# Kernel optimization log

Measured on AMD Instinct MI355X. Metric: run time of the kernel, lower is better.

## Reference

```python
import jax, jax.numpy as jnp
import numpy as np

D_MODEL = 1024
HEAD = 16
D_K = D_MODEL // HEAD
NEG_INF = -1.0e9


def setup_inputs() -> dict:
    key = jax.random.key(0)
    ks = jax.random.split(key, 12)
    B, S = 2, 2048
    scale = 1.0 / np.sqrt(D_MODEL)
    inp = {
        "query": jax.random.normal(ks[0], (B, S, D_MODEL), jnp.float32),
        "key": jax.random.normal(ks[1], (B, S, D_MODEL), jnp.float32),
        "value": jax.random.normal(ks[2], (B, S, D_MODEL), jnp.float32),
        "mask": jax.random.randint(ks[3], (B, 1, 1, S), 0, 2, jnp.int32),
        "Wq": jax.random.normal(ks[4], (D_MODEL, D_MODEL), jnp.float32) * scale,
        "bq": jnp.zeros((D_MODEL,), jnp.float32),
        "Wk": jax.random.normal(ks[5], (D_MODEL, D_MODEL), jnp.float32) * scale,
        "bk": jnp.zeros((D_MODEL,), jnp.float32),
        "Wv": jax.random.normal(ks[6], (D_MODEL, D_MODEL), jnp.float32) * scale,
        "bv": jnp.zeros((D_MODEL,), jnp.float32),
        "Wo": jax.random.normal(ks[7], (D_MODEL, D_MODEL), jnp.float32) * scale,
        "bo": jnp.zeros((D_MODEL,), jnp.float32),
    }
    return inp


def reference(query, key, value, mask, Wq, bq, Wk, bk, Wv, bv, Wo, bo):
    B, S, _ = query.shape
    # QKV projections (torch nn.Linear: x @ W^T + b)
    q = query @ Wq.T + bq
    k = key @ Wk.T + bk
    v = value @ Wv.T + bv
    # [B, H, S, d_k]
    q = q.reshape(B, S, HEAD, D_K).transpose(0, 2, 1, 3)
    k = k.reshape(B, S, HEAD, D_K).transpose(0, 2, 1, 3)
    v = v.reshape(B, S, HEAD, D_K).transpose(0, 2, 1, 3)
    # scores [B, H, S, S]
    scores = jnp.einsum("bhqd,bhkd->bhqk", q, k) / jnp.sqrt(jnp.float32(D_K))
    scores = jnp.where(mask == 0, jnp.float32(NEG_INF), scores)
    attn = jax.nn.softmax(scores, axis=-1)  # dropout off (eval mode)
    ctx = jnp.einsum("bhqk,bhkd->bhqd", attn, v)
    ctx = ctx.transpose(0, 2, 1, 3).reshape(B, S, D_MODEL)
    return ctx @ Wo.T + bo
```

## Files before the change

kernel.cpp:

```cpp
#include <hip/hip_runtime.h>
#include <cstdint>
#include <cstddef>

typedef unsigned short u16;
typedef unsigned int   u32;
typedef __bf16 bf16x8 __attribute__((ext_vector_type(8)));
typedef float  f32x4  __attribute__((ext_vector_type(4)));

#define D_MODEL 1024
#define SEQ     2048
#define NTOK    4096
#define NHEAD   16
#define DK      64

__device__ __forceinline__ float fast_exp2(float x) {
  return __builtin_amdgcn_exp2f(x);
}

__device__ __forceinline__ u16 f2bf(float f) {
  u32 u = __builtin_bit_cast(u32, f);
  u += 0x7fffu + ((u >> 16) & 1u);
  return (u16)(u >> 16);
}

__device__ __forceinline__ void gload16(const u16* g, u16* l) {
  __builtin_amdgcn_global_load_lds(
      (__attribute__((address_space(1))) void*)(uintptr_t)g,
      (__attribute__((address_space(3))) void*)l,
      16, 0, 0);
}

__global__ __launch_bounds__(256) void mask_scan(const int* __restrict__ mask,
                                                 int* __restrict__ idx,
                                                 int* __restrict__ cnt) {
  const int b = blockIdx.x, t = threadIdx.x;
  const int lane = t & 63, w = t >> 6;
  __shared__ int sW[4];
  __shared__ int sTot;
  int m8[8];
  const int base = b * SEQ + t * 8;
  int tot = 0;
#pragma unroll
  for (int i = 0; i < 8; ++i) {
    m8[i] = (mask[base + i] != 0);
    tot += m8[i];
  }
  int v = tot;
#pragma unroll
  for (int d = 1; d < 64; d <<= 1) {
    int u = __shfl_up(v, d);
    if (lane >= d) v += u;
  }
  if (lane == 63) sW[w] = v;
  __syncthreads();
  if (t == 0) {
    int run = 0;
#pragma unroll
    for (int i = 0; i < 4; ++i) { int tmp = sW[i]; sW[i] = run; run += tmp; }
    sTot = run;
  }
  __syncthreads();
  int pos = v - tot + sW[w];
#pragma unroll
  for (int i = 0; i < 8; ++i)
    if (m8[i]) idx[b * SEQ + pos++] = t * 8 + i;
  const int cn = sTot;
  if (t == 0) cnt[b] = cn;
  for (int j = cn + t; j < SEQ; j += 256) idx[b * SEQ + j] = 0;
}

__global__ __launch_bounds__(256) void w_convert(
    const float* __restrict__ wq, const float* __restrict__ wk,
    const float* __restrict__ wv, const float* __restrict__ wo,
    u16* __restrict__ wb) {
  const int total = 1 << 20;
  for (int cid = blockIdx.x * blockDim.x + threadIdx.x; cid < total;
       cid += gridDim.x * blockDim.x) {
    int which = cid >> 18;
    int off = cid & ((1 << 18) - 1);
    const float* src = which == 0 ? wq : (which == 1 ? wk : (which == 2 ? wv : wo));
    u16* dst = wb + ((size_t)which << 20);
    float4 f = ((const float4*)src)[off];
    ushort4 u;
    u.x = f2bf(f.x); u.y = f2bf(f.y); u.z = f2bf(f.z); u.w = f2bf(f.w);
    ((ushort4*)dst)[off] = u;
  }
}

__global__ __launch_bounds__(256, 3) void gemm_qkv(
    const float* __restrict__ Aq, const float* __restrict__ Ak,
    const float* __restrict__ Av, const u16* __restrict__ Bw,
    const float* __restrict__ b0, const float* __restrict__ b1,
    const float* __restrict__ b2, u16* __restrict__ Cout) {
  __shared__ __align__(16) u16 smem[3 * 128 * 64];
  u16* sA = smem;

  const int t = threadIdx.x;
  const int z = blockIdx.z;
  const float* Ap = (z == 0) ? Aq : ((z == 1) ? Ak : Av);
  const u16* Bp = Bw + ((size_t)z << 20);
  const float* bias = (z == 0) ? b0 : ((z == 1) ? b1 : b2);
  const float scl = (z == 0) ? 0.18033688011f : 1.0f;

  const int m0 = blockIdx.x * 128, n0 = blockIdx.y * 128;
  const int lane = t & 63, wv = t >> 6;
  const int wm = (wv >> 1) * 64, wn = (wv & 1) * 64;
  const int c = lane & 15, qd = lane >> 4;

  const int arow = t >> 3;
  const int aoff = (((t & 7) - arow) & 7) * 8;
  const float* gaA = Ap + (size_t)(m0 + arow) * D_MODEL + aoff;
  const u16* gaB = Bp + (size_t)(n0 + arow) * D_MODEL + aoff;

  float4 pa[4][2];
#pragma unroll
  for (int j = 0; j < 4; ++j) {
    pa[j][0] = *(const float4*)(gaA + (size_t)(32 * j) * D_MODEL);
    pa[j][1] = *(const float4*)(gaA + (size_t)(32 * j) * D_MODEL + 4);
  }
#pragma unroll
  for (int j = 0; j < 4; ++j)
    gload16(gaB + (size_t)(32 * j) * D_MODEL, smem + 8192 + (t + 256 * j) * 8);

  f32x4 acc[4][4] = {};

  for (int kbi = 0; kbi < 16; ++kbi) {
    const int cur = kbi & 1;
    __syncthreads();
#pragma unroll
    for (int j = 0; j < 4; ++j) {
      u32 w[4];
#pragma unroll
      for (int h2 = 0; h2 < 2; ++h2) {
        float4 f = pa[j][h2];
        w[2 * h2] = (u32)f2bf(f.x) | ((u32)f2bf(f.y) << 16);
        w[2 * h2 + 1] = (u32)f2bf(f.z) | ((u32)f2bf(f.w) << 16);
      }
      uint4 v4 = {w[0], w[1], w[2], w[3]};
      *(uint4*)&sA[(t + 256 * j) * 8] = v4;
    }
    __syncthreads();
    if (kbi + 1 < 16) {
      const int kb2 = (kbi + 1) * 64;
      u16* sBn = smem + 8192 + (1 - cur) * 8192;
#pragma unroll
      for (int j = 0; j < 4; ++j)
        gload16(gaB + kb2 + (size_t)(32 * j) * D_MODEL, sBn + (t + 256 * j) * 8);
#pragma unroll
      for (int j = 0; j < 4; ++j) {
        pa[j][0] = *(const float4*)(gaA + kb2 + (size_t)(32 * j) * D_MODEL);
        pa[j][1] = *(const float4*)(gaA + kb2 + (size_t)(32 * j) * D_MODEL + 4);
      }
    }
    const u16* sB = smem + 8192 + cur * 8192;
#pragma unroll
    for (int s = 0; s < 2; ++s) {
      const int ao = ((s * 4 + qd + wm + c) & 7) * 8;
      const int bo = ((s * 4 + qd + wn + c) & 7) * 8;
      bf16x8 af[4], bfr[4];
#pragma unroll
      for (int i = 0; i < 4; ++i)
        af[i] = *(const bf16x8*)&sA[(wm + i * 16 + c) * 64 + ao];
#pragma unroll
      for (int j = 0; j < 4; ++j)
        bfr[j] = *(const bf16x8*)&sB[(wn + j * 16 + c) * 64 + bo];
#pragma unroll
      for (int i = 0; i < 4; ++i)
#pragma unroll
        for (int j = 0; j < 4; ++j)
          acc[i][j] = __builtin_amdgcn_mfma_f32_16x16x32_bf16(af[i], bfr[j],
                                                              acc[i][j], 0, 0, 0);
    }
  }
  __syncthreads();

  u16* sC = smem;
  if (z == 2) {
#pragma unroll
    for (int j = 0; j < 4; ++j) {
      const int col = wn + j * 16 + c;
      const float bv = bias[n0 + col];
#pragma unroll
      for (int i = 0; i < 4; ++i)
#pragma unroll
        for (int r = 0; r < 4; ++r)
          sC[col * 136 + wm + i * 16 + qd * 4 + r] = f2bf(acc[i][j][r] + bv);
    }
    __syncthreads();
    u16* VT = Cout + ((size_t)2 << 22);
    const int bb = m0 >> 11, s0 = m0 & 2047;
    const int sidx = (t & 15) * 8;
#pragma unroll
    for (int outer = 0; outer < 8; ++outer) {
      const int vrow = outer * 16 + (t >> 4);
      const int col = n0 + vrow;
      const int hh = col >> 6, dd = col & 63;
      uint4 val = *(const uint4*)&sC[vrow * 136 + sidx];
      *(uint4*)&VT[((size_t)((bb * NHEAD + hh) * DK + dd)) * SEQ + s0 + sidx] =
          val;
    }
  } else {
#pragma unroll
    for (int j = 0; j < 4; ++j) {
      const int col = wn + j * 16 + c;
      const float bv = bias[n0 + col];
#pragma unroll
      for (int i = 0; i < 4; ++i)
#pragma unroll
        for (int r = 0; r < 4; ++r)
          sC[(wm + i * 16 + qd * 4 + r) * 136 + col] =
              f2bf((acc[i][j][r] + bv) * scl);
    }
    __syncthreads();
    u16* outp = Cout + ((size_t)z << 22);
    const int cidx = (t & 15) * 8;
#pragma unroll
    for (int outer = 0; outer < 8; ++outer) {
      const int lrow = outer * 16 + (t >> 4);
      uint4 val = *(const uint4*)&sC[lrow * 136 + cidx];
      *(uint4*)&outp[(size_t)(m0 + lrow) * D_MODEL + n0 + cidx] = val;
    }
  }
}

__global__ __launch_bounds__(256) void vtc_gather(const u16* __restrict__ VT,
                                                  const int* __restrict__ idx,
                                                  const int* __restrict__ cnt,
                                                  u16* __restrict__ VTc) {
  const int row = blockIdx.x;
  const int b = row >> 10;
  const int cn = cnt[b];
  const u16* src = VT + (size_t)row * SEQ;
  u16* dst = VTc + (size_t)row * SEQ;
  const int* ib = idx + b * SEQ;
  for (int j = threadIdx.x; j < cn; j += 256) dst[j] = src[ib[j]];
}

__global__ __launch_bounds__(256) void mha_attn(
    const u16* __restrict__ QKVb, const u16* __restrict__ VTc,
    const int* __restrict__ idx, const int* __restrict__ cnt,
    u16* __restrict__ Opart, float* __restrict__ ml) {
  __shared__ __align__(16) u16 sK[64 * 72];
  __shared__ __align__(16) u16 sVt[64 * 72];
  __shared__ __align__(16) u16 sP[128 * 72];

  const int t = threadIdx.x, lane = t & 63, wq = t >> 6;
  const int c = lane & 15, qd = lane >> 4;
  const int qb = blockIdx.x, h = blockIdx.y;
  const int b = blockIdx.z & 1, ck = blockIdx.z >> 1;

  const int cn = cnt[b];
  const int nb = (cn + 63) >> 6;
  const int half = (nb + 1) >> 1;
  const int kstart = ck ? half : 0;
  const int kend = ck ? nb : half;

  const u16* Qg = QKVb;
  const u16* Kg = QKVb + ((size_t)4 << 20);
  const u16* VTch = VTc + ((size_t)((b * NHEAD + h) * DK)) * SEQ;
  const int rowbase = b * SEQ;
  const int colbase = h * DK;

  bf16x8 aq[2][2];
#pragma unroll
  for (int qt = 0; qt < 2; ++qt) {
    const u16* g = Qg +
                   (size_t)(rowbase + qb * 128 + wq * 32 + qt * 16 + c) * D_MODEL +
                   colbase + qd * 8;
    aq[qt][0] = *(const bf16x8*)g;
    aq[qt][1] = *(const bf16x8*)(g + 32);
  }

  float l[2] = {0.f, 0.f};
  f32x4 o[2][4] = {};
  const float MADD = -1.4426950e9f;
  const float MFIX = 16.0f;

  const int r0s = t >> 2, offs = (t & 3) * 16;
  const u16* gvb = VTch + (size_t)r0s * SEQ + offs;
  const int* idxb = idx + b * SEQ + r0s;

  uint4 k0, k1, v0, v1;
  int sNext2 = 0;
  if (kstart < kend) {
    const int s0i = idxb[kstart * 64];
    const u16* gk = Kg + (size_t)(rowbase + s0i) * D_MODEL + colbase + offs;
    const u16* gv = gvb + kstart * 64;
    k0 = *(const uint4*)gk;
    k1 = *(const uint4*)(gk + 8);
    v0 = *(const uint4*)gv;
    v1 = *(const uint4*)(gv + 8);
    if (kstart + 1 < kend) sNext2 = idxb[(kstart + 1) * 64];
  }

  for (int kbi = kstart; kbi < kend; ++kbi) {
    __syncthreads();
    *(uint4*)&sK[r0s * 72 + offs] = k0;
    *(uint4*)&sK[r0s * 72 + offs + 8] = k1;
    *(uint4*)&sVt[r0s * 72 + offs] = v0;
    *(uint4*)&sVt[r0s * 72 + offs + 8] = v1;
    __syncthreads();
    if (kbi + 1 < kend) {
      const u16* gk = Kg + (size_t)(rowbase + sNext2) * D_MODEL + colbase + offs;
      const u16* gv = gvb + (kbi + 1) * 64;
      k0 = *(const uint4*)gk;
      k1 = *(const uint4*)(gk + 8);
      v0 = *(const uint4*)gv;
      v1 = *(const uint4*)(gv + 8);
    }
    if (kbi + 2 < kend) sNext2 = idxb[(kbi + 2) * 64];

    const bool full = ((kbi + 1) << 6) <= cn;
    f32x4 st[2][4];
#pragma unroll
    for (int tt = 0; tt < 4; ++tt) {
      bf16x8 ak0 = *(const bf16x8*)&sK[(tt * 16 + c) * 72 + qd * 8];
      bf16x8 ak1 = *(const bf16x8*)&sK[(tt * 16 + c) * 72 + qd * 8 + 32];
      f32x4 cin;
      if (full) {
        cin = f32x4{0.f, 0.f, 0.f, 0.f};
      } else {
        const int jb = (kbi << 6) + tt * 16 + qd * 4;
        cin = f32x4{jb + 0 < cn ? 0.f : MADD, jb + 1 < cn ? 0.f : MADD,
                    jb + 2 < cn ? 0.f : MADD, jb + 3 < cn ? 0.f : MADD};
      }
#pragma unroll
      for (int qt = 0; qt < 2; ++qt) {
        f32x4 a =
            __builtin_amdgcn_mfma_f32_16x16x32_bf16(ak0, aq[qt][0], cin, 0, 0, 0);
        a = __builtin_amdgcn_mfma_f32_16x16x32_bf16(ak1, aq[qt][1], a, 0, 0, 0);
        st[qt][tt] = a;
      }
    }

#pragma unroll
    for (int qt = 0; qt < 2; ++qt) {
      float sum = 0.f;
      const int prow = (wq * 32 + qt * 16 + c) * 72;
#pragma unroll
      for (int tt = 0; tt < 4; ++tt) {
        u32 pk[2];
#pragma unroll
        for (int pr = 0; pr < 2; ++pr) {
          u32 p0 = __builtin_bit_cast(u32, fast_exp2(st[qt][tt][2 * pr] - MFIX));
          u32 p1 =
              __builtin_bit_cast(u32, fast_exp2(st[qt][tt][2 * pr + 1] - MFIX));
          u32 hi1 = p1 & 0xffff0000u;
          pk[pr] = (p0 >> 16) | hi1;
          sum += __builtin_bit_cast(float, p0 & 0xffff0000u);
          sum += __builtin_bit_cast(float, hi1);
        }
        uint2 pv2 = {pk[0], pk[1]};
        *(uint2*)&sP[prow + tt * 16 + qd * 4] = pv2;
      }
      l[qt] += sum;
    }

    bf16x8 bp[2][2];
#pragma unroll
    for (int qt = 0; qt < 2; ++qt) {
      const int prow = (wq * 32 + qt * 16 + c) * 72;
      bp[qt][0] = *(const bf16x8*)&sP[prow + qd * 8];
      bp[qt][1] = *(const bf16x8*)&sP[prow + qd * 8 + 32];
    }
#pragma unroll
    for (int dt = 0; dt < 4; ++dt) {
      bf16x8 av0 = *(const bf16x8*)&sVt[(dt * 16 + c) * 72 + qd * 8];
      bf16x8 av1 = *(const bf16x8*)&sVt[(dt * 16 + c) * 72 + qd * 8 + 32];
#pragma unroll
      for (int qt = 0; qt < 2; ++qt) {
        o[qt][dt] =
            __builtin_amdgcn_mfma_f32_16x16x32_bf16(av0, bp[qt][0], o[qt][dt], 0, 0, 0);
        o[qt][dt] =
            __builtin_amdgcn_mfma_f32_16x16x32_bf16(av1, bp[qt][1], o[qt][dt], 0, 0, 0);
      }
    }
  }

  const size_t obase =
      (size_t)ck * 4194304 + ((size_t)((b * NHEAD + h) * SEQ) + qb * 128) * 64;
  const int mlbase = ((ck * 2 + b) * NHEAD + h) * SEQ + qb * 128;
#pragma unroll
  for (int qt = 0; qt < 2; ++qt) {
    float ls = l[qt];
    ls += __shfl_xor(ls, 16);
    ls += __shfl_xor(ls, 32);
    const float inv = (ls != 0.f) ? 1.0f / ls : 0.f;
    const int q = wq * 32 + qt * 16 + c;
#pragma unroll
    for (int dt = 0; dt < 4; ++dt) {
      u32 lo = (u32)f2bf(o[qt][dt][0] * inv) |
               ((u32)f2bf(o[qt][dt][1] * inv) << 16);
      u32 hi = (u32)f2bf(o[qt][dt][2] * inv) |
               ((u32)f2bf(o[qt][dt][3] * inv) << 16);
      uint2 ov = {lo, hi};
      *(uint2*)&Opart[obase + (size_t)q * 64 + dt * 16 + qd * 4] = ov;
    }
    if (qd == 0) ml[mlbase + q] = ls;
  }
}

__global__ __launch_bounds__(256) void mha_combine(
    const u16* __restrict__ Opart, const float* __restrict__ ml,
    u16* __restrict__ ctx) {
  const int tid = blockIdx.x * 256 + threadIdx.x;
  const int row = tid >> 3, d0 = (tid & 7) * 8;
  const int b = row >> 15, h = (row >> 11) & 15, q = row & 2047;
  float l1 = ml[row];
  float l2 = ml[65536 + row];
  float inv = 1.0f / (l1 + l2);
  float w1 = l1 * inv, w2 = l2 * inv;
  const size_t o1 = (size_t)row * 64 + d0;
  uint4 pa = *(const uint4*)(Opart + o1);
  uint4 pb = *(const uint4*)(Opart + 4194304 + o1);
  u32 wa[4] = {pa.x, pa.y, pa.z, pa.w};
  u32 wb[4] = {pb.x, pb.y, pb.z, pb.w};
  u32 out[4];
#pragma unroll
  for (int j = 0; j < 4; ++j) {
    float alo = __builtin_bit_cast(float, wa[j] << 16);
    float ahi = __builtin_bit_cast(float, wa[j] & 0xffff0000u);
    float blo = __builtin_bit_cast(float, wb[j] << 16);
    float bhi = __builtin_bit_cast(float, wb[j] & 0xffff0000u);
    float rlo = w1 * alo + w2 * blo;
    float rhi = w1 * ahi + w2 * bhi;
    out[j] = (u32)f2bf(rlo) | ((u32)f2bf(rhi) << 16);
  }
  uint4 ov = {out[0], out[1], out[2], out[3]};
  *(uint4*)&ctx[((size_t)(b * SEQ + q)) * D_MODEL + h * DK + d0] = ov;
}

__global__ __launch_bounds__(256) void gemm_out(
    const u16* __restrict__ A, const u16* __restrict__ Bw,
    const float* __restrict__ bias, float* __restrict__ Cout) {
  __shared__ __align__(16) u16 sAb[2][128 * 64];
  __shared__ __align__(16) u16 sBc[2][64 * 64];

  const int t = threadIdx.x;
  const int m0 = blockIdx.x * 128, n0 = blockIdx.y * 64;
  const int lane = t & 63, wv = t >> 6;
  const int wm = (wv >> 1) * 64, wn = (wv & 1) * 32;
  const int c = lane & 15, qd = lane >> 4;

  const int arow = t >> 3;
  const int aoff = (((t & 7) - arow) & 7) * 8;
  const u16* gaA = A + (size_t)(m0 + arow) * D_MODEL + aoff;
  const u16* gaB = Bw + (size_t)(n0 + arow) * D_MODEL + aoff;

#pragma unroll
  for (int j = 0; j < 4; ++j)
    gload16(gaA + (size_t)(32 * j) * D_MODEL, &sAb[0][(t + 256 * j) * 8]);
#pragma unroll
  for (int j = 0; j < 2; ++j)
    gload16(gaB + (size_t)(32 * j) * D_MODEL, &sBc[0][(t + 256 * j) * 8]);

  f32x4 acc[4][2] = {};

  for (int kbi = 0; kbi < 16; ++kbi) {
    const int cur = kbi & 1;
    __syncthreads();
    if (kbi + 1 < 16) {
      const int kb2 = (kbi + 1) * 64;
#pragma unroll
      for (int j = 0; j < 4; ++j)
        gload16(gaA + kb2 + (size_t)(32 * j) * D_MODEL,
                &sAb[1 - cur][(t + 256 * j) * 8]);
#pragma unroll
      for (int j = 0; j < 2; ++j)
        gload16(gaB + kb2 + (size_t)(32 * j) * D_MODEL,
                &sBc[1 - cur][(t + 256 * j) * 8]);
    }
    const u16* sA = sAb[cur];
    const u16* sB = sBc[cur];
#pragma unroll
    for (int s = 0; s < 2; ++s) {
      const int ao = ((s * 4 + qd + wm + c) & 7) * 8;
      const int bo = ((s * 4 + qd + wn + c) & 7) * 8;
      bf16x8 af[4], bfr[2];
#pragma unroll
      for (int i = 0; i < 4; ++i)
        af[i] = *(const bf16x8*)&sA[(wm + i * 16 + c) * 64 + ao];
#pragma unroll
      for (int j = 0; j < 2; ++j)
        bfr[j] = *(const bf16x8*)&sB[(wn + j * 16 + c) * 64 + bo];
#pragma unroll
      for (int i = 0; i < 4; ++i)
#pragma unroll
        for (int j = 0; j < 2; ++j)
          acc[i][j] = __builtin_amdgcn_mfma_f32_16x16x32_bf16(af[i], bfr[j],
                                                              acc[i][j], 0, 0, 0);
    }
  }

#pragma unroll
  for (int j = 0; j < 2; ++j) {
    const int col = n0 + wn + j * 16 + c;
    const float bv = bias[col];
#pragma unroll
    for (int i = 0; i < 4; ++i)
#pragma unroll
      for (int r = 0; r < 4; ++r) {
        const int row = m0 + wm + i * 16 + qd * 4 + r;
        Cout[(size_t)row * D_MODEL + col] = acc[i][j][r] + bv;
      }
  }
}

extern "C" void kernel_launch(void* const* d_in, const int* in_sizes, int n_in,
                              void* d_out, int out_size, void* d_ws,
                              size_t ws_size, hipStream_t stream) {
  const float* query = (const float*)d_in[0];
  const float* key   = (const float*)d_in[1];
  const float* value = (const float*)d_in[2];
  const int*   mask  = (const int*)d_in[3];
  const float* Wq = (const float*)d_in[4];
  const float* bq = (const float*)d_in[5];
  const float* Wk = (const float*)d_in[6];
  const float* bk = (const float*)d_in[7];
  const float* Wv = (const float*)d_in[8];
  const float* bv = (const float*)d_in[9];
  const float* Wo = (const float*)d_in[10];
  const float* bo = (const float*)d_in[11];

  u16* ws  = (u16*)d_ws;
  u16* Wb  = ws + ((size_t)12 << 20);
  u16* QKV = ws + ((size_t)16 << 20);
  u16* CTX = ws + ((size_t)28 << 20);
  u16* VTc = ws;
  u16* Opart = ws + ((size_t)4 << 20);
  float* ml = (float*)(ws + ((size_t)12 << 20));
  int* idxp = (int*)(ws + ((size_t)28 << 20));
  int* cntp = idxp + 2 * SEQ;

  mask_scan<<<dim3(2), dim3(256), 0, stream>>>(mask, idxp, cntp);
  w_convert<<<dim3(1024), dim3(256), 0, stream>>>(Wq, Wk, Wv, Wo, Wb);
  gemm_qkv<<<dim3(32, 8, 3), dim3(256), 0, stream>>>(query, key, value, Wb, bq,
                                                     bk, bv, QKV);
  vtc_gather<<<dim3(2048), dim3(256), 0, stream>>>(QKV + ((size_t)8 << 20), idxp,
                                                   cntp, VTc);
  mha_attn<<<dim3(16, 16, 4), dim3(256), 0, stream>>>(QKV, VTc, idxp, cntp,
                                                      Opart, ml);
  mha_combine<<<dim3(2048), dim3(256), 0, stream>>>(Opart, ml, CTX);
  gemm_out<<<dim3(32, 16), dim3(256), 0, stream>>>(CTX, Wb + ((size_t)3 << 20),
                                                   bo, (float*)d_out);
}
```

Before: 214.0 us.

## Fuse mask scan with weight convert; load QKV A-operand directly into registers

Merges the mask prefix-scan and weight bf16 conversion into one launch, removing one kernel launch. In gemm_qkv, each lane now loads its fp32 A fragment straight from global memory in MFMA operand layout and converts it in registers. This drops the A tile from shared memory along with one barrier per k-step, and shrinks LDS to the B double buffer. The cost is more registers per thread (occupancy hint lowered from 3 to 2) and global A loads that are less coalesced.

```diff
diff --git a/kernel.cpp b/kernel.cpp
--- a/kernel.cpp
+++ b/kernel.cpp
@@ -30,70 +30,70 @@
       16, 0, 0);
 }
 
-__global__ __launch_bounds__(256) void mask_scan(const int* __restrict__ mask,
-                                                 int* __restrict__ idx,
-                                                 int* __restrict__ cnt) {
-  const int b = blockIdx.x, t = threadIdx.x;
-  const int lane = t & 63, w = t >> 6;
-  __shared__ int sW[4];
-  __shared__ int sTot;
-  int m8[8];
-  const int base = b * SEQ + t * 8;
-  int tot = 0;
-#pragma unroll
-  for (int i = 0; i < 8; ++i) {
-    m8[i] = (mask[base + i] != 0);
-    tot += m8[i];
-  }
-  int v = tot;
-#pragma unroll
-  for (int d = 1; d < 64; d <<= 1) {
-    int u = __shfl_up(v, d);
-    if (lane >= d) v += u;
-  }
-  if (lane == 63) sW[w] = v;
-  __syncthreads();
-  if (t == 0) {
-    int run = 0;
-#pragma unroll
-    for (int i = 0; i < 4; ++i) { int tmp = sW[i]; sW[i] = run; run += tmp; }
-    sTot = run;
-  }
-  __syncthreads();
-  int pos = v - tot + sW[w];
-#pragma unroll
-  for (int i = 0; i < 8; ++i)
-    if (m8[i]) idx[b * SEQ + pos++] = t * 8 + i;
-  const int cn = sTot;
-  if (t == 0) cnt[b] = cn;
-  for (int j = cn + t; j < SEQ; j += 256) idx[b * SEQ + j] = 0;
-}
-
-__global__ __launch_bounds__(256) void w_convert(
-    const float* __restrict__ wq, const float* __restrict__ wk,
-    const float* __restrict__ wv, const float* __restrict__ wo,
-    u16* __restrict__ wb) {
-  const int total = 1 << 20;
-  for (int cid = blockIdx.x * blockDim.x + threadIdx.x; cid < total;
-       cid += gridDim.x * blockDim.x) {
-    int which = cid >> 18;
-    int off = cid & ((1 << 18) - 1);
-    const float* src = which == 0 ? wq : (which == 1 ? wk : (which == 2 ? wv : wo));
-    u16* dst = wb + ((size_t)which << 20);
-    float4 f = ((const float4*)src)[off];
-    ushort4 u;
-    u.x = f2bf(f.x); u.y = f2bf(f.y); u.z = f2bf(f.z); u.w = f2bf(f.w);
-    ((ushort4*)dst)[off] = u;
-  }
-}
-
-__global__ __launch_bounds__(256, 3) void gemm_qkv(
+__global__ __launch_bounds__(256) void prep(
+    const int* __restrict__ mask, const float* __restrict__ wq,
+    const float* __restrict__ wk, const float* __restrict__ wv,
+    const float* __restrict__ wo, u16* __restrict__ wb,
+    int* __restrict__ idx, int* __restrict__ cnt) {
+  const int t = threadIdx.x;
+  if (blockIdx.x < 2) {
+    const int b = blockIdx.x;
+    const int lane = t & 63, w = t >> 6;
+    __shared__ int sW[4];
+    __shared__ int sTot;
+    int m8[8];
+    const int base = b * SEQ + t * 8;
+    int tot = 0;
+#pragma unroll
+    for (int i = 0; i < 8; ++i) {
+      m8[i] = (mask[base + i] != 0);
+      tot += m8[i];
+    }
+    int v = tot;
+#pragma unroll
+    for (int d = 1; d < 64; d <<= 1) {
+      int u = __shfl_up(v, d);
+      if (lane >= d) v += u;
+    }
+    if (lane == 63) sW[w] = v;
+    __syncthreads();
+    if (t == 0) {
+      int run = 0;
+#pragma unroll
+      for (int i = 0; i < 4; ++i) { int tmp = sW[i]; sW[i] = run; run += tmp; }
+      sTot = run;
+    }
+    __syncthreads();
+    int pos = v - tot + sW[w];
+#pragma unroll
+    for (int i = 0; i < 8; ++i)
+      if (m8[i]) idx[b * SEQ + pos++] = t * 8 + i;
+    const int cn = sTot;
+    if (t == 0) cnt[b] = cn;
+    for (int j = cn + t; j < SEQ; j += 256) idx[b * SEQ + j] = 0;
+  } else {
+    const int total = 1 << 20;
+    const int stride = (gridDim.x - 2) * 256;
+    for (int cid = (blockIdx.x - 2) * 256 + t; cid < total; cid += stride) {
+      int which = cid >> 18;
+      int off = cid & ((1 << 18) - 1);
+      const float* src =
+          which == 0 ? wq : (which == 1 ? wk : (which == 2 ? wv : wo));
+      u16* dst = wb + ((size_t)which << 20);
+      float4 f = ((const float4*)src)[off];
+      ushort4 u;
+      u.x = f2bf(f.x); u.y = f2bf(f.y); u.z = f2bf(f.z); u.w = f2bf(f.w);
+      ((ushort4*)dst)[off] = u;
+    }
+  }
+}
+
+__global__ __launch_bounds__(256, 2) void gemm_qkv(
     const float* __restrict__ Aq, const float* __restrict__ Ak,
     const float* __restrict__ Av, const u16* __restrict__ Bw,
     const float* __restrict__ b0, const float* __restrict__ b1,
     const float* __restrict__ b2, u16* __restrict__ Cout) {
-  __shared__ __align__(16) u16 smem[3 * 128 * 64];
-  u16* sA = smem;
+  __shared__ __align__(16) u16 smem[128 * 136];
 
   const int t = threadIdx.x;
   const int z = blockIdx.z;
@@ -107,60 +107,59 @@
   const int wm = (wv >> 1) * 64, wn = (wv & 1) * 64;
   const int c = lane & 15, qd = lane >> 4;
 
-  const int arow = t >> 3;
-  const int aoff = (((t & 7) - arow) & 7) * 8;
-  const float* gaA = Ap + (size_t)(m0 + arow) * D_MODEL + aoff;
-  const u16* gaB = Bp + (size_t)(n0 + arow) * D_MODEL + aoff;
-
-  float4 pa[4][2];
-#pragma unroll
-  for (int j = 0; j < 4; ++j) {
-    pa[j][0] = *(const float4*)(gaA + (size_t)(32 * j) * D_MODEL);
-    pa[j][1] = *(const float4*)(gaA + (size_t)(32 * j) * D_MODEL + 4);
+  const int brow = t >> 3;
+  const int boff = (((t & 7) - brow) & 7) * 8;
+  const u16* gaB = Bp + (size_t)(n0 + brow) * D_MODEL + boff;
+
+  const float* gA = Ap + (size_t)(m0 + wm + c) * D_MODEL + qd * 8;
+
+  float4 pa[8][2];
+#pragma unroll
+  for (int f = 0; f < 8; ++f) {
+    const float* p = gA + (f >> 1) * (16 * D_MODEL) + (f & 1) * 32;
+    pa[f][0] = *(const float4*)p;
+    pa[f][1] = *(const float4*)(p + 4);
   }
 #pragma unroll
   for (int j = 0; j < 4; ++j)
-    gload16(gaB + (size_t)(32 * j) * D_MODEL, smem + 8192 + (t + 256 * j) * 8);
+    gload16(gaB + (size_t)(32 * j) * D_MODEL, smem + (t + 256 * j) * 8);
 
   f32x4 acc[4][4] = {};
 
   for (int kbi = 0; kbi < 16; ++kbi) {
     const int cur = kbi & 1;
     __syncthreads();
-#pragma unroll
-    for (int j = 0; j < 4; ++j) {
-      u32 w[4];
-#pragma unroll
-      for (int h2 = 0; h2 < 2; ++h2) {
-        float4 f = pa[j][h2];
-        w[2 * h2] = (u32)f2bf(f.x) | ((u32)f2bf(f.y) << 16);
-        w[2 * h2 + 1] = (u32)f2bf(f.z) | ((u32)f2bf(f.w) << 16);
-      }
-      uint4 v4 = {w[0], w[1], w[2], w[3]};
-      *(uint4*)&sA[(t + 256 * j) * 8] = v4;
-    }
-    __syncthreads();
+    if (kbi + 1 < 16) {
+      u16* sBn = smem + (1 - cur) * 8192;
+#pragma unroll
+      for (int j = 0; j < 4; ++j)
+        gload16(gaB + (kbi + 1) * 64 + (size_t)(32 * j) * D_MODEL,
+                sBn + (t + 256 * j) * 8);
+    }
+    bf16x8 af[8];
+#pragma unroll
+    for (int f = 0; f < 8; ++f) {
+      u32 w0 = (u32)f2bf(pa[f][0].x) | ((u32)f2bf(pa[f][0].y) << 16);
+      u32 w1 = (u32)f2bf(pa[f][0].z) | ((u32)f2bf(pa[f][0].w) << 16);
+      u32 w2 = (u32)f2bf(pa[f][1].x) | ((u32)f2bf(pa[f][1].y) << 16);
+      u32 w3 = (u32)f2bf(pa[f][1].z) | ((u32)f2bf(pa[f][1].w) << 16);
+      uint4 u4 = {w0, w1, w2, w3};
+      af[f] = __builtin_bit_cast(bf16x8, u4);
+    }
     if (kbi + 1 < 16) {
       const int kb2 = (kbi + 1) * 64;
-      u16* sBn = smem + 8192 + (1 - cur) * 8192;
-#pragma unroll
-      for (int j = 0; j < 4; ++j)
-        gload16(gaB + kb2 + (size_t)(32 * j) * D_MODEL, sBn + (t + 256 * j) * 8);
-#pragma unroll
-      for (int j = 0; j < 4; ++j) {
-        pa[j][0] = *(const float4*)(gaA + kb2 + (size_t)(32 * j) * D_MODEL);
-        pa[j][1] = *(const float4*)(gaA + kb2 + (size_t)(32 * j) * D_MODEL + 4);
+#pragma unroll
+      for (int f = 0; f < 8; ++f) {
+        const float* p = gA + kb2 + (f >> 1) * (16 * D_MODEL) + (f & 1) * 32;
+        pa[f][0] = *(const float4*)p;
+        pa[f][1] = *(const float4*)(p + 4);
       }
     }
-    const u16* sB = smem + 8192 + cur * 8192;
+    const u16* sB = smem + cur * 8192;
 #pragma unroll
     for (int s = 0; s < 2; ++s) {
-      const int ao = ((s * 4 + qd + wm + c) & 7) * 8;
       const int bo = ((s * 4 + qd + wn + c) & 7) * 8;
-      bf16x8 af[4], bfr[4];
-#pragma unroll
-      for (int i = 0; i < 4; ++i)
-        af[i] = *(const bf16x8*)&sA[(wm + i * 16 + c) * 64 + ao];
+      bf16x8 bfr[4];
 #pragma unroll
       for (int j = 0; j < 4; ++j)
         bfr[j] = *(const bf16x8*)&sB[(wn + j * 16 + c) * 64 + bo];
@@ -168,8 +167,8 @@
       for (int i = 0; i < 4; ++i)
 #pragma unroll
         for (int j = 0; j < 4; ++j)
-          acc[i][j] = __builtin_amdgcn_mfma_f32_16x16x32_bf16(af[i], bfr[j],
-                                                              acc[i][j], 0, 0, 0);
+          acc[i][j] = __builtin_amdgcn_mfma_f32_16x16x32_bf16(
+              af[i * 2 + s], bfr[j], acc[i][j], 0, 0, 0);
     }
   }
   __syncthreads();
@@ -532,8 +531,8 @@
   int* idxp = (int*)(ws + ((size_t)28 << 20));
   int* cntp = idxp + 2 * SEQ;
 
-  mask_scan<<<dim3(2), dim3(256), 0, stream>>>(mask, idxp, cntp);
-  w_convert<<<dim3(1024), dim3(256), 0, stream>>>(Wq, Wk, Wv, Wo, Wb);
+  prep<<<dim3(1026), dim3(256), 0, stream>>>(mask, Wq, Wk, Wv, Wo, Wb, idxp,
+                                             cntp);
   gemm_qkv<<<dim3(32, 8, 3), dim3(256), 0, stream>>>(query, key, value, Wb, bq,
                                                      bk, bv, QKV);
   vtc_gather<<<dim3(2048), dim3(256), 0, stream>>>(QKV + ((size_t)8 << 20), idxp,
```

New measurement: 277.0 us. +29.5%, slower.

## Fuse mask scan with weight convert and scatter compacted V in QKV epilogue

Applied to the files above, without the earlier changes.

Merges the mask prefix-scan and weight bf16 conversion into one prep kernel, which also emits a per-position rank array. The V projection epilogue then writes transposed V straight into compacted positions using mask and rank, so the separate vtc_gather kernel and its extra read and write pass are removed. The cost is two fewer launches traded for scalar 2-byte scattered stores and per-element mask/rank loads in the GEMM epilogue, in place of 16-byte vector stores. Workspace offsets are rearranged to match.

```diff
diff --git a/kernel.cpp b/kernel.cpp
--- a/kernel.cpp
+++ b/kernel.cpp
@@ -30,60 +30,63 @@
       16, 0, 0);
 }
 
-__global__ __launch_bounds__(256) void mask_scan(const int* __restrict__ mask,
-                                                 int* __restrict__ idx,
-                                                 int* __restrict__ cnt) {
-  const int b = blockIdx.x, t = threadIdx.x;
-  const int lane = t & 63, w = t >> 6;
-  __shared__ int sW[4];
-  __shared__ int sTot;
-  int m8[8];
-  const int base = b * SEQ + t * 8;
-  int tot = 0;
-#pragma unroll
-  for (int i = 0; i < 8; ++i) {
-    m8[i] = (mask[base + i] != 0);
-    tot += m8[i];
-  }
-  int v = tot;
-#pragma unroll
-  for (int d = 1; d < 64; d <<= 1) {
-    int u = __shfl_up(v, d);
-    if (lane >= d) v += u;
-  }
-  if (lane == 63) sW[w] = v;
-  __syncthreads();
-  if (t == 0) {
-    int run = 0;
-#pragma unroll
-    for (int i = 0; i < 4; ++i) { int tmp = sW[i]; sW[i] = run; run += tmp; }
-    sTot = run;
-  }
-  __syncthreads();
-  int pos = v - tot + sW[w];
-#pragma unroll
-  for (int i = 0; i < 8; ++i)
-    if (m8[i]) idx[b * SEQ + pos++] = t * 8 + i;
-  const int cn = sTot;
-  if (t == 0) cnt[b] = cn;
-  for (int j = cn + t; j < SEQ; j += 256) idx[b * SEQ + j] = 0;
-}
-
-__global__ __launch_bounds__(256) void w_convert(
-    const float* __restrict__ wq, const float* __restrict__ wk,
-    const float* __restrict__ wv, const float* __restrict__ wo,
-    u16* __restrict__ wb) {
-  const int total = 1 << 20;
-  for (int cid = blockIdx.x * blockDim.x + threadIdx.x; cid < total;
-       cid += gridDim.x * blockDim.x) {
-    int which = cid >> 18;
-    int off = cid & ((1 << 18) - 1);
-    const float* src = which == 0 ? wq : (which == 1 ? wk : (which == 2 ? wv : wo));
-    u16* dst = wb + ((size_t)which << 20);
-    float4 f = ((const float4*)src)[off];
-    ushort4 u;
-    u.x = f2bf(f.x); u.y = f2bf(f.y); u.z = f2bf(f.z); u.w = f2bf(f.w);
-    ((ushort4*)dst)[off] = u;
+__global__ __launch_bounds__(256) void prep(
+    const int* __restrict__ mask, const float* __restrict__ wq,
+    const float* __restrict__ wk, const float* __restrict__ wv,
+    const float* __restrict__ wo, u16* __restrict__ wb,
+    int* __restrict__ idx, int* __restrict__ rank, int* __restrict__ cnt) {
+  const int t = threadIdx.x;
+  if (blockIdx.x < 2) {
+    const int b = blockIdx.x;
+    const int lane = t & 63, w = t >> 6;
+    __shared__ int sW[4];
+    __shared__ int sTot;
+    int m8[8];
+    const int base = b * SEQ + t * 8;
+    int tot = 0;
+#pragma unroll
+    for (int i = 0; i < 8; ++i) {
+      m8[i] = (mask[base + i] != 0);
+      tot += m8[i];
+    }
+    int v = tot;
+#pragma unroll
+    for (int d = 1; d < 64; d <<= 1) {
+      int u = __shfl_up(v, d);
+      if (lane >= d) v += u;
+    }
+    if (lane == 63) sW[w] = v;
+    __syncthreads();
+    if (t == 0) {
+      int run = 0;
+#pragma unroll
+      for (int i = 0; i < 4; ++i) { int tmp = sW[i]; sW[i] = run; run += tmp; }
+      sTot = run;
+    }
+    __syncthreads();
+    int pos = v - tot + sW[w];
+#pragma unroll
+    for (int i = 0; i < 8; ++i) {
+      rank[b * SEQ + t * 8 + i] = pos;
+      if (m8[i]) { idx[b * SEQ + pos] = t * 8 + i; ++pos; }
+    }
+    const int cn = sTot;
+    if (t == 0) cnt[b] = cn;
+    for (int j = cn + t; j < SEQ; j += 256) idx[b * SEQ + j] = 0;
+  } else {
+    const int total = 1 << 20;
+    const int stride = (gridDim.x - 2) * 256;
+    for (int cid = (blockIdx.x - 2) * 256 + t; cid < total; cid += stride) {
+      int which = cid >> 18;
+      int off = cid & ((1 << 18) - 1);
+      const float* src =
+          which == 0 ? wq : (which == 1 ? wk : (which == 2 ? wv : wo));
+      u16* dst = wb + ((size_t)which << 20);
+      float4 f = ((const float4*)src)[off];
+      ushort4 u;
+      u.x = f2bf(f.x); u.y = f2bf(f.y); u.z = f2bf(f.z); u.w = f2bf(f.w);
+      ((ushort4*)dst)[off] = u;
+    }
   }
 }
 
@@ -91,7 +94,8 @@
     const float* __restrict__ Aq, const float* __restrict__ Ak,
     const float* __restrict__ Av, const u16* __restrict__ Bw,
     const float* __restrict__ b0, const float* __restrict__ b1,
-    const float* __restrict__ b2, u16* __restrict__ Cout) {
+    const float* __restrict__ b2, const int* __restrict__ mask,
+    const int* __restrict__ rank, u16* __restrict__ Cout) {
   __shared__ __align__(16) u16 smem[3 * 128 * 64];
   u16* sA = smem;
 
@@ -187,17 +191,20 @@
           sC[col * 136 + wm + i * 16 + qd * 4 + r] = f2bf(acc[i][j][r] + bv);
     }
     __syncthreads();
-    u16* VT = Cout + ((size_t)2 << 22);
+    u16* VTc = Cout + ((size_t)2 << 22);
     const int bb = m0 >> 11, s0 = m0 & 2047;
     const int sidx = (t & 15) * 8;
+    const int sg = bb * SEQ + s0 + sidx;
 #pragma unroll
     for (int outer = 0; outer < 8; ++outer) {
       const int vrow = outer * 16 + (t >> 4);
       const int col = n0 + vrow;
       const int hh = col >> 6, dd = col & 63;
-      uint4 val = *(const uint4*)&sC[vrow * 136 + sidx];
-      *(uint4*)&VT[((size_t)((bb * NHEAD + hh) * DK + dd)) * SEQ + s0 + sidx] =
-          val;
+      const u16* src = &sC[vrow * 136 + sidx];
+      u16* dstrow = VTc + ((size_t)((bb * NHEAD + hh) * DK + dd)) * SEQ;
+#pragma unroll
+      for (int i = 0; i < 8; ++i)
+        if (mask[sg + i] != 0) dstrow[rank[sg + i]] = src[i];
     }
   } else {
 #pragma unroll
@@ -223,23 +230,10 @@
   }
 }
 
-__global__ __launch_bounds__(256) void vtc_gather(const u16* __restrict__ VT,
-                                                  const int* __restrict__ idx,
-                                                  const int* __restrict__ cnt,
-                                                  u16* __restrict__ VTc) {
-  const int row = blockIdx.x;
-  const int b = row >> 10;
-  const int cn = cnt[b];
-  const u16* src = VT + (size_t)row * SEQ;
-  u16* dst = VTc + (size_t)row * SEQ;
-  const int* ib = idx + b * SEQ;
-  for (int j = threadIdx.x; j < cn; j += 256) dst[j] = src[ib[j]];
-}
-
 __global__ __launch_bounds__(256) void mha_attn(
-    const u16* __restrict__ QKVb, const u16* __restrict__ VTc,
-    const int* __restrict__ idx, const int* __restrict__ cnt,
-    u16* __restrict__ Opart, float* __restrict__ ml) {
+    const u16* __restrict__ QKVb, const int* __restrict__ idx,
+    const int* __restrict__ cnt, u16* __restrict__ Opart,
+    float* __restrict__ ml) {
   __shared__ __align__(16) u16 sK[64 * 72];
   __shared__ __align__(16) u16 sVt[64 * 72];
   __shared__ __align__(16) u16 sP[128 * 72];
@@ -257,7 +251,8 @@
 
   const u16* Qg = QKVb;
   const u16* Kg = QKVb + ((size_t)4 << 20);
-  const u16* VTch = VTc + ((size_t)((b * NHEAD + h) * DK)) * SEQ;
+  const u16* VTch = QKVb + ((size_t)8 << 20) +
+                    ((size_t)((b * NHEAD + h) * DK)) * SEQ;
   const int rowbase = b * SEQ;
   const int colbase = h * DK;
 
@@ -523,23 +518,21 @@
   const float* bo = (const float*)d_in[11];
 
   u16* ws  = (u16*)d_ws;
+  u16* Opart = ws;
+  float* ml = (float*)(ws + ((size_t)8 << 20));
   u16* Wb  = ws + ((size_t)12 << 20);
   u16* QKV = ws + ((size_t)16 << 20);
   u16* CTX = ws + ((size_t)28 << 20);
-  u16* VTc = ws;
-  u16* Opart = ws + ((size_t)4 << 20);
-  float* ml = (float*)(ws + ((size_t)12 << 20));
   int* idxp = (int*)(ws + ((size_t)28 << 20));
-  int* cntp = idxp + 2 * SEQ;
-
-  mask_scan<<<dim3(2), dim3(256), 0, stream>>>(mask, idxp, cntp);
-  w_convert<<<dim3(1024), dim3(256), 0, stream>>>(Wq, Wk, Wv, Wo, Wb);
+  int* rankp = idxp + 2 * SEQ;
+  int* cntp = rankp + 2 * SEQ;
+
+  prep<<<dim3(1026), dim3(256), 0, stream>>>(mask, Wq, Wk, Wv, Wo, Wb, idxp,
+                                             rankp, cntp);
   gemm_qkv<<<dim3(32, 8, 3), dim3(256), 0, stream>>>(query, key, value, Wb, bq,
-                                                     bk, bv, QKV);
-  vtc_gather<<<dim3(2048), dim3(256), 0, stream>>>(QKV + ((size_t)8 << 20), idxp,
-                                                   cntp, VTc);
-  mha_attn<<<dim3(16, 16, 4), dim3(256), 0, stream>>>(QKV, VTc, idxp, cntp,
-                                                      Opart, ml);
+                                                     bk, bv, mask, rankp, QKV);
+  mha_attn<<<dim3(16, 16, 4), dim3(256), 0, stream>>>(QKV, idxp, cntp, Opart,
+                                                      ml);
   mha_combine<<<dim3(2048), dim3(256), 0, stream>>>(Opart, ml, CTX);
   gemm_out<<<dim3(32, 16), dim3(256), 0, stream>>>(CTX, Wb + ((size_t)3 << 20),
                                                    bo, (float*)d_out);
```

New measurement: 217.9 us. No clear change (+1.9%).

## Fuse split-softmax combine into output GEMM and merge prep kernels

Applied to the files above, without the earlier changes.

Removes the separate combine kernel by having the output GEMM read the two attention partials and their row sums directly, merging them into the A tile in shared memory each k-step. The mask scan and weight conversion kernels are merged into one launch. The bf16 rounding is simplified to round-half-up. This eliminates the CTX write/read and two launches, but each N-block redundantly re-reads both partials and redoes the combine, with synchronous register-staged A loads and an extra barrier per iteration.

```diff
diff --git a/kernel.cpp b/kernel.cpp
--- a/kernel.cpp
+++ b/kernel.cpp
@@ -19,8 +19,7 @@
 
 __device__ __forceinline__ u16 f2bf(float f) {
   u32 u = __builtin_bit_cast(u32, f);
-  u += 0x7fffu + ((u >> 16) & 1u);
-  return (u16)(u >> 16);
+  return (u16)((u + 0x8000u) >> 16);
 }
 
 __device__ __forceinline__ void gload16(const u16* g, u16* l) {
@@ -30,60 +29,61 @@
       16, 0, 0);
 }
 
-__global__ __launch_bounds__(256) void mask_scan(const int* __restrict__ mask,
-                                                 int* __restrict__ idx,
-                                                 int* __restrict__ cnt) {
-  const int b = blockIdx.x, t = threadIdx.x;
-  const int lane = t & 63, w = t >> 6;
-  __shared__ int sW[4];
-  __shared__ int sTot;
-  int m8[8];
-  const int base = b * SEQ + t * 8;
-  int tot = 0;
-#pragma unroll
-  for (int i = 0; i < 8; ++i) {
-    m8[i] = (mask[base + i] != 0);
-    tot += m8[i];
-  }
-  int v = tot;
-#pragma unroll
-  for (int d = 1; d < 64; d <<= 1) {
-    int u = __shfl_up(v, d);
-    if (lane >= d) v += u;
-  }
-  if (lane == 63) sW[w] = v;
-  __syncthreads();
-  if (t == 0) {
-    int run = 0;
-#pragma unroll
-    for (int i = 0; i < 4; ++i) { int tmp = sW[i]; sW[i] = run; run += tmp; }
-    sTot = run;
-  }
-  __syncthreads();
-  int pos = v - tot + sW[w];
-#pragma unroll
-  for (int i = 0; i < 8; ++i)
-    if (m8[i]) idx[b * SEQ + pos++] = t * 8 + i;
-  const int cn = sTot;
-  if (t == 0) cnt[b] = cn;
-  for (int j = cn + t; j < SEQ; j += 256) idx[b * SEQ + j] = 0;
-}
-
-__global__ __launch_bounds__(256) void w_convert(
-    const float* __restrict__ wq, const float* __restrict__ wk,
-    const float* __restrict__ wv, const float* __restrict__ wo,
-    u16* __restrict__ wb) {
-  const int total = 1 << 20;
-  for (int cid = blockIdx.x * blockDim.x + threadIdx.x; cid < total;
-       cid += gridDim.x * blockDim.x) {
-    int which = cid >> 18;
-    int off = cid & ((1 << 18) - 1);
-    const float* src = which == 0 ? wq : (which == 1 ? wk : (which == 2 ? wv : wo));
-    u16* dst = wb + ((size_t)which << 20);
-    float4 f = ((const float4*)src)[off];
-    ushort4 u;
-    u.x = f2bf(f.x); u.y = f2bf(f.y); u.z = f2bf(f.z); u.w = f2bf(f.w);
-    ((ushort4*)dst)[off] = u;
+__global__ __launch_bounds__(256) void prep(
+    const int* __restrict__ mask, const float* __restrict__ wq,
+    const float* __restrict__ wk, const float* __restrict__ wv,
+    const float* __restrict__ wo, u16* __restrict__ wb,
+    int* __restrict__ idx, int* __restrict__ cnt) {
+  const int t = threadIdx.x;
+  if (blockIdx.x < 2) {
+    const int b = blockIdx.x;
+    const int lane = t & 63, w = t >> 6;
+    __shared__ int sW[4];
+    __shared__ int sTot;
+    int m8[8];
+    const int base = b * SEQ + t * 8;
+    int tot = 0;
+#pragma unroll
+    for (int i = 0; i < 8; ++i) {
+      m8[i] = (mask[base + i] != 0);
+      tot += m8[i];
+    }
+    int v = tot;
+#pragma unroll
+    for (int d = 1; d < 64; d <<= 1) {
+      int u = __shfl_up(v, d);
+      if (lane >= d) v += u;
+    }
+    if (lane == 63) sW[w] = v;
+    __syncthreads();
+    if (t == 0) {
+      int run = 0;
+#pragma unroll
+      for (int i = 0; i < 4; ++i) { int tmp = sW[i]; sW[i] = run; run += tmp; }
+      sTot = run;
+    }
+    __syncthreads();
+    int pos = v - tot + sW[w];
+#pragma unroll
+    for (int i = 0; i < 8; ++i)
+      if (m8[i]) idx[b * SEQ + pos++] = t * 8 + i;
+    const int cn = sTot;
+    if (t == 0) cnt[b] = cn;
+    for (int j = cn + t; j < SEQ; j += 256) idx[b * SEQ + j] = 0;
+  } else {
+    const int total = 1 << 20;
+    const int stride = (gridDim.x - 2) * 256;
+    for (int cid = (blockIdx.x - 2) * 256 + t; cid < total; cid += stride) {
+      int which = cid >> 18;
+      int off = cid & ((1 << 18) - 1);
+      const float* src =
+          which == 0 ? wq : (which == 1 ? wk : (which == 2 ? wv : wo));
+      u16* dst = wb + ((size_t)which << 20);
+      float4 f = ((const float4*)src)[off];
+      ushort4 u;
+      u.x = f2bf(f.x); u.y = f2bf(f.y); u.z = f2bf(f.z); u.w = f2bf(f.w);
+      ((ushort4*)dst)[off] = u;
+    }
   }
 }
 
@@ -400,78 +400,86 @@
   }
 }
 
-__global__ __launch_bounds__(256) void mha_combine(
+__global__ __launch_bounds__(256, 2) void gemm_out(
     const u16* __restrict__ Opart, const float* __restrict__ ml,
-    u16* __restrict__ ctx) {
-  const int tid = blockIdx.x * 256 + threadIdx.x;
-  const int row = tid >> 3, d0 = (tid & 7) * 8;
-  const int b = row >> 15, h = (row >> 11) & 15, q = row & 2047;
-  float l1 = ml[row];
-  float l2 = ml[65536 + row];
-  float inv = 1.0f / (l1 + l2);
-  float w1 = l1 * inv, w2 = l2 * inv;
-  const size_t o1 = (size_t)row * 64 + d0;
-  uint4 pa = *(const uint4*)(Opart + o1);
-  uint4 pb = *(const uint4*)(Opart + 4194304 + o1);
-  u32 wa[4] = {pa.x, pa.y, pa.z, pa.w};
-  u32 wb[4] = {pb.x, pb.y, pb.z, pb.w};
-  u32 out[4];
-#pragma unroll
-  for (int j = 0; j < 4; ++j) {
-    float alo = __builtin_bit_cast(float, wa[j] << 16);
-    float ahi = __builtin_bit_cast(float, wa[j] & 0xffff0000u);
-    float blo = __builtin_bit_cast(float, wb[j] << 16);
-    float bhi = __builtin_bit_cast(float, wb[j] & 0xffff0000u);
-    float rlo = w1 * alo + w2 * blo;
-    float rhi = w1 * ahi + w2 * bhi;
-    out[j] = (u32)f2bf(rlo) | ((u32)f2bf(rhi) << 16);
-  }
-  uint4 ov = {out[0], out[1], out[2], out[3]};
-  *(uint4*)&ctx[((size_t)(b * SEQ + q)) * D_MODEL + h * DK + d0] = ov;
-}
-
-__global__ __launch_bounds__(256) void gemm_out(
-    const u16* __restrict__ A, const u16* __restrict__ Bw,
-    const float* __restrict__ bias, float* __restrict__ Cout) {
-  __shared__ __align__(16) u16 sAb[2][128 * 64];
-  __shared__ __align__(16) u16 sBc[2][64 * 64];
+    const u16* __restrict__ Bw, const float* __restrict__ bias,
+    float* __restrict__ Cout) {
+  __shared__ __align__(16) u16 smem[2 * 64 * 64 + 128 * 64];
 
   const int t = threadIdx.x;
   const int m0 = blockIdx.x * 128, n0 = blockIdx.y * 64;
   const int lane = t & 63, wv = t >> 6;
   const int wm = (wv >> 1) * 64, wn = (wv & 1) * 32;
   const int c = lane & 15, qd = lane >> 4;
+  u16* sA = smem + 8192;
 
   const int arow = t >> 3;
   const int aoff = (((t & 7) - arow) & 7) * 8;
-  const u16* gaA = A + (size_t)(m0 + arow) * D_MODEL + aoff;
-  const u16* gaB = Bw + (size_t)(n0 + arow) * D_MODEL + aoff;
-
-#pragma unroll
-  for (int j = 0; j < 4; ++j)
-    gload16(gaA + (size_t)(32 * j) * D_MODEL, &sAb[0][(t + 256 * j) * 8]);
+  const int bb = m0 >> 11, s0 = m0 & 2047;
+  const int r2base = bb * NHEAD * SEQ + s0 + arow;
+
+  const int brow = t >> 3;
+  const int boff = (((t & 7) - brow) & 7) * 8;
+  const u16* gaB = Bw + (size_t)(n0 + brow) * D_MODEL + boff;
+
+  uint4 po1[4], po2[4];
+  float pl1[4], pl2[4];
+#pragma unroll
+  for (int j = 0; j < 4; ++j) {
+    const int r2 = r2base + 32 * j;
+    po1[j] = *(const uint4*)(Opart + (size_t)r2 * 64 + aoff);
+    po2[j] = *(const uint4*)(Opart + 4194304 + (size_t)r2 * 64 + aoff);
+    pl1[j] = ml[r2];
+    pl2[j] = ml[r2 + 65536];
+  }
 #pragma unroll
   for (int j = 0; j < 2; ++j)
-    gload16(gaB + (size_t)(32 * j) * D_MODEL, &sBc[0][(t + 256 * j) * 8]);
+    gload16(gaB + (size_t)(32 * j) * D_MODEL, smem + (t + 256 * j) * 8);
 
   f32x4 acc[4][2] = {};
 
   for (int kbi = 0; kbi < 16; ++kbi) {
     const int cur = kbi & 1;
     __syncthreads();
+#pragma unroll
+    for (int j = 0; j < 4; ++j) {
+      const float inv = 1.0f / (pl1[j] + pl2[j]);
+      const float w1 = pl1[j] * inv, w2 = pl2[j] * inv;
+      u32 a4[4] = {po1[j].x, po1[j].y, po1[j].z, po1[j].w};
+      u32 b4[4] = {po2[j].x, po2[j].y, po2[j].z, po2[j].w};
+      u32 wo[4];
+#pragma unroll
+      for (int p = 0; p < 4; ++p) {
+        float alo = __builtin_bit_cast(float, a4[p] << 16);
+        float ahi = __builtin_bit_cast(float, a4[p] & 0xffff0000u);
+        float blo = __builtin_bit_cast(float, b4[p] << 16);
+        float bhi = __builtin_bit_cast(float, b4[p] & 0xffff0000u);
+        float rlo = w1 * alo + w2 * blo;
+        float rhi = w1 * ahi + w2 * bhi;
+        wo[p] = (u32)f2bf(rlo) | ((u32)f2bf(rhi) << 16);
+      }
+      uint4 v4 = {wo[0], wo[1], wo[2], wo[3]};
+      *(uint4*)&sA[(t + 256 * j) * 8] = v4;
+    }
+    __syncthreads();
     if (kbi + 1 < 16) {
       const int kb2 = (kbi + 1) * 64;
-#pragma unroll
-      for (int j = 0; j < 4; ++j)
-        gload16(gaA + kb2 + (size_t)(32 * j) * D_MODEL,
-                &sAb[1 - cur][(t + 256 * j) * 8]);
+      u16* sBn = smem + (1 - cur) * 8192 / 2;
 #pragma unroll
       for (int j = 0; j < 2; ++j)
         gload16(gaB + kb2 + (size_t)(32 * j) * D_MODEL,
-                &sBc[1 - cur][(t + 256 * j) * 8]);
-    }
-    const u16* sA = sAb[cur];
-    const u16* sB = sBc[cur];
+                smem + (1 - cur) * 4096 + (t + 256 * j) * 8);
+      (void)sBn;
+#pragma unroll
+      for (int j = 0; j < 4; ++j) {
+        const int r2 = r2base + (kbi + 1) * SEQ + 32 * j;
+        po1[j] = *(const uint4*)(Opart + (size_t)r2 * 64 + aoff);
+        po2[j] = *(const uint4*)(Opart + 4194304 + (size_t)r2 * 64 + aoff);
+        pl1[j] = ml[r2];
+        pl2[j] = ml[r2 + 65536];
+      }
+    }
+    const u16* sB = smem + cur * 4096;
 #pragma unroll
     for (int s = 0; s < 2; ++s) {
       const int ao = ((s * 4 + qd + wm + c) & 7) * 8;
@@ -523,24 +531,23 @@
   const float* bo = (const float*)d_in[11];
 
   u16* ws  = (u16*)d_ws;
-  u16* Wb  = ws + ((size_t)12 << 20);
-  u16* QKV = ws + ((size_t)16 << 20);
-  u16* CTX = ws + ((size_t)28 << 20);
   u16* VTc = ws;
   u16* Opart = ws + ((size_t)4 << 20);
+  u16* Wb  = ws + ((size_t)12 << 20);
   float* ml = (float*)(ws + ((size_t)12 << 20));
+  u16* QKV = ws + ((size_t)16 << 20);
   int* idxp = (int*)(ws + ((size_t)28 << 20));
   int* cntp = idxp + 2 * SEQ;
 
-  mask_scan<<<dim3(2), dim3(256), 0, stream>>>(mask, idxp, cntp);
-  w_convert<<<dim3(1024), dim3(256), 0, stream>>>(Wq, Wk, Wv, Wo, Wb);
+  prep<<<dim3(1026), dim3(256), 0, stream>>>(mask, Wq, Wk, Wv, Wo, Wb, idxp,
+                                             cntp);
   gemm_qkv<<<dim3(32, 8, 3), dim3(256), 0, stream>>>(query, key, value, Wb, bq,
                                                      bk, bv, QKV);
   vtc_gather<<<dim3(2048), dim3(256), 0, stream>>>(QKV + ((size_t)8 << 20), idxp,
                                                    cntp, VTc);
   mha_attn<<<dim3(16, 16, 4), dim3(256), 0, stream>>>(QKV, VTc, idxp, cntp,
                                                       Opart, ml);
-  mha_combine<<<dim3(2048), dim3(256), 0, stream>>>(Opart, ml, CTX);
-  gemm_out<<<dim3(32, 16), dim3(256), 0, stream>>>(CTX, Wb + ((size_t)3 << 20),
-                                                   bo, (float*)d_out);
-}
+  gemm_out<<<dim3(32, 16), dim3(256), 0, stream>>>(Opart, ml,
+                                                   Wb + ((size_t)3 << 20), bo,
+                                                   (float*)d_out);
+}
```

Measured after the change: 215.4 us. About the same (+0.7%).
